# Performance work log

Hardware: AMD Instinct MI355X
Metric: run time of the kernel (lower is better)

Reference implementation:

```python
import jax, jax.numpy as jnp
import numpy as np

B, S, D = 4, 2048, 1024  # batch, seq_len, d_model (d_in == d_model)


def setup_inputs() -> dict:
    key = jax.random.key(0)
    ks = jax.random.split(key, 9)
    scale = 1.0 / np.sqrt(D)
    return {
        "q": jax.random.normal(ks[0], (B, S, D), jnp.float32),
        "k": jax.random.normal(ks[1], (B, S, D), jnp.float32),
        "v": jax.random.normal(ks[2], (B, S, D), jnp.float32),
        "Wq": jax.random.normal(ks[3], (D, D), jnp.float32) * scale,
        "bq": jnp.zeros((D,), jnp.float32),
        "Wk": jax.random.normal(ks[4], (D, D), jnp.float32) * scale,
        "bk": jnp.zeros((D,), jnp.float32),
        "Wv": jax.random.normal(ks[5], (D, D), jnp.float32) * scale,
        "bv": jnp.zeros((D,), jnp.float32),
    }


def reference(q, k, v, Wq, bq, Wk, bk, Wv, bv):
    query = q @ Wq + bq                      # [B, S, D]
    key_p = k @ Wk + bk                      # [B, S, D]
    value = v @ Wv + bv                      # [B, S, D]
    inv_sqrt_d = 1.0 / jnp.sqrt(jnp.asarray(D, query.dtype))
    scores = jnp.einsum('bqd,bkd->bqk', query, key_p) * inv_sqrt_d  # [B, S, S]
    w = jax.nn.softmax(scores, axis=-1)
    return jnp.einsum('bqk,bkd->bqd', w, value)  # [B, S, D]
```

## Files before the change

### kernel.cpp

```cpp
#include <hip/hip_runtime.h>
#include <math.h>


using short8  = __attribute__((ext_vector_type(8))) short;
using floatx4 = __attribute__((ext_vector_type(4))) float;

__device__ __forceinline__ unsigned short f2bf(float f) {
    union { float f; unsigned u; } x; x.f = f;
    return (unsigned short)((x.u + 0x8000u) >> 16);
}

__device__ __forceinline__ void gload_lds16(const unsigned short* g, unsigned short* l) {
    __builtin_amdgcn_global_load_lds(
        (const __attribute__((address_space(1))) unsigned int*)g,
        (__attribute__((address_space(3))) unsigned int*)l, 16, 0, 0);
}

#define SBAR   __builtin_amdgcn_s_barrier()
#define LGKM0  asm volatile("s_waitcnt lgkmcnt(0)" ::: "memory")
#define VMW(n) asm volatile("s_waitcnt vmcnt(" #n ")" ::: "memory")

__global__ __launch_bounds__(256) void prep(
    const float* __restrict__ q, const float* __restrict__ k, const float* __restrict__ v,
    const float* __restrict__ W0, const float* __restrict__ W1, const float* __restrict__ W2,
    unsigned short* __restrict__ qkvbf, unsigned short* __restrict__ Wt)
{
    __shared__ float tile[32][33];
    const int id = blockIdx.x;
    const int t  = threadIdx.x;
    if (id < 24576) {
        const int z  = id >> 13;
        const int xb = id & 8191;
        const float* x = (z == 0) ? q : (z == 1) ? k : v;
        const size_t i = ((size_t)xb * 256 + t) * 4;
        const float4 a = *(const float4*)(x + i);
        ushort4 p = { f2bf(a.x), f2bf(a.y), f2bf(a.z), f2bf(a.w) };
        *(ushort4*)(qkvbf + (size_t)z * 8192 * 1024 + i) = p;
    } else {
        const int idt = id - 24576;
        const int z  = idt >> 10;
        const int r  = idt & 1023;
        const int bx = (r & 31) * 32;
        const int by = (r >> 5) * 32;
        const float* W = (z == 0) ? W0 : (z == 1) ? W1 : W2;
        unsigned short* o = Wt + (size_t)z * 1024 * 1024;
        const int tx = t & 31;
        const int ty = (t >> 5) * 4;
        #pragma unroll
        for (int rr = 0; rr < 4; ++rr)
            tile[ty + rr][tx] = W[(size_t)(by + ty + rr) * 1024 + bx + tx];
        __syncthreads();
        #pragma unroll
        for (int rr = 0; rr < 4; ++rr)
            o[(size_t)(bx + ty + rr) * 1024 + by + tx] = f2bf(tile[tx][ty + rr]);
    }
}


#define STAGE_A(bb, kh, tt) do { \
    gload_lds16(gA + (size_t)srowA * lda + (tt) * 64 + (kh) * 32 + scol, \
                lds + (bb) * 24576 + (kh) * 4096 + t512 * 8); \
} while (0)

#define STAGE_B(bb, kh, tt) do { \
    const unsigned short* s_ = gB + (size_t)srowA * ldb + (tt) * 64 + (kh) * 32 + scol; \
    unsigned short* d_ = lds + (bb) * 24576 + 8192 + (kh) * 8192 + t512 * 8; \
    gload_lds16(s_, d_); \
    gload_lds16(s_ + (size_t)128 * ldb, d_ + 4096); \
} while (0)

#define LDSA(bb, kh, i) (*(const short8*)&lds[(bb) * 24576 + (kh) * 4096 + (arow + (i) * 16) * 32 + rslot])
#define LDSB(bb, kh, j) (*(const short8*)&lds[(bb) * 24576 + 8192 + (kh) * 8192 + (brow + (j) * 16) * 32 + rslot])

#define MFMA16 do { \
    __builtin_amdgcn_s_setprio(1); \
    _Pragma("unroll") \
    for (int i_ = 0; i_ < 4; ++i_) \
        _Pragma("unroll") \
        for (int j_ = 0; j_ < 4; ++j_) \
            acc[i_][j_] = __builtin_amdgcn_mfma_f32_16x16x32_bf16( \
                af[i_], bf[j_], acc[i_][j_], 0, 0, 0); \
    __builtin_amdgcn_s_setprio(0); \
} while (0)

__device__ __forceinline__ void gemm2ph(
    const unsigned short* __restrict__ gA, int lda,
    const unsigned short* __restrict__ gB, int ldb,
    int nt, unsigned short* lds, floatx4 (&acc)[4][4])
{
    const int t512 = threadIdx.x;
    const int lane = t512 & 63;
    const int wave = t512 >> 6;
    const int wr   = wave >> 2;
    const int wc   = wave & 3;
    const int l15  = lane & 15;
    const int quad = lane >> 4;
    const int srowA = t512 >> 2;
    const int scol  = ((t512 & 3) ^ ((t512 >> 3) & 3)) * 8;
    const int rslot = (quad ^ ((l15 >> 1) & 3)) * 8;
    const int arow  = wr * 64 + l15;
    const int brow  = wc * 64 + l15;

    short8 af[4], bf[4];

    STAGE_A(0, 0, 0); STAGE_B(0, 0, 0);
    STAGE_A(0, 1, 0); STAGE_B(0, 1, 0);
    STAGE_A(1, 0, 1); STAGE_B(1, 0, 1);
    VMW(6);
    SBAR;

    int b = 0;
    for (int t = 0; t < nt; ++t, b ^= 1) {
        #pragma unroll
        for (int j = 0; j < 4; ++j) bf[j] = LDSB(b, 0, j);
        #pragma unroll
        for (int i = 0; i < 4; ++i) af[i] = LDSA(b, 0, i);
        if (t + 1 < nt) { STAGE_A(b ^ 1, 1, t + 1); STAGE_B(b ^ 1, 1, t + 1); }
        SBAR; LGKM0;
        MFMA16;
        if (t < nt - 1) VMW(6); else VMW(0);
        SBAR;
        #pragma unroll
        for (int j = 0; j < 4; ++j) bf[j] = LDSB(b, 1, j);
        #pragma unroll
        for (int i = 0; i < 4; ++i) af[i] = LDSA(b, 1, i);
        if (t + 2 < nt) { STAGE_A(b, 0, t + 2); STAGE_B(b, 0, t + 2); }
        SBAR; LGKM0;
        MFMA16;
        if (t < nt - 1) {
            if (t + 2 < nt) VMW(6); else VMW(3);
            SBAR;
        }
    }
}

#define EPI_IDS                                   \
    const int tt   = threadIdx.x;                 \
    const int lane = tt & 63;                     \
    const int wave = tt >> 6;                     \
    const int wr   = wave >> 2;                   \
    const int wc   = wave & 3;                    \
    const int l15  = lane & 15;                   \
    const int quad = lane >> 4;

__global__ __launch_bounds__(512) void proj8(
    const unsigned short* __restrict__ Abf,
    const unsigned short* __restrict__ Wt,
    const float* __restrict__ bq, const float* __restrict__ bk, const float* __restrict__ bv,
    unsigned short* __restrict__ Qp, unsigned short* __restrict__ Kp,
    unsigned short* __restrict__ Vpt)
{
    __shared__ __attribute__((aligned(16))) unsigned short lds[49152];
    const int id = blockIdx.x;
    const int g  = (id & 7) * 96 + (id >> 3);
    const int z  = g >> 8;
    const int r  = g & 255;
    const int m0 = (r >> 2) * 128;
    const int n0 = (r & 3) * 256;

    const unsigned short* gA = Abf + (size_t)z * 8192 * 1024 + (size_t)m0 * 1024;
    const unsigned short* gB = Wt  + (size_t)z * 1024 * 1024 + (size_t)n0 * 1024;

    floatx4 acc[4][4] = {};
    gemm2ph(gA, 1024, gB, 1024, 16, lds, acc);

    EPI_IDS
    const float* bias = (z == 0) ? bq : (z == 1) ? bk : bv;
    #pragma unroll
    for (int j = 0; j < 4; ++j) {
        const int col = n0 + wc * 64 + j * 16 + l15;
        const float bv_ = bias[col];
        #pragma unroll
        for (int i = 0; i < 4; ++i) {
            const int row = m0 + wr * 64 + i * 16 + quad * 4;
            if (z < 2) {
                unsigned short* C = (z == 0) ? Qp : Kp;
                #pragma unroll
                for (int r2 = 0; r2 < 4; ++r2)
                    C[(size_t)(row + r2) * 1024 + col] = f2bf(acc[i][j][r2] + bv_);
            } else {
                ushort4 p = { f2bf(acc[i][j][0] + bv_), f2bf(acc[i][j][1] + bv_),
                              f2bf(acc[i][j][2] + bv_), f2bf(acc[i][j][3] + bv_) };
                *(ushort4*)&Vpt[(size_t)col * 8192 + row] = p;
            }
        }
    }
}

__global__ __launch_bounds__(512) void scores8(
    const unsigned short* __restrict__ Qp,
    const unsigned short* __restrict__ Kp,
    unsigned short* __restrict__ Pexp,
    float* __restrict__ rowsum)
{
    __shared__ __attribute__((aligned(16))) unsigned short lds[49152];
    const int id = blockIdx.x;
    const int g  = (id & 7) * 64 + (id >> 3);
    const int z  = g >> 7;
    const int r  = g & 127;
    const int m0 = (r >> 3) * 128;
    const int n0 = (r & 7) * 256;

    const unsigned short* gA = Qp + (size_t)z * 2048 * 1024 + (size_t)m0 * 1024;
    const unsigned short* gB = Kp + (size_t)z * 2048 * 1024 + (size_t)n0 * 1024;

    floatx4 acc[4][4] = {};
    gemm2ph(gA, 1024, gB, 1024, 16, lds, acc);

    EPI_IDS
    unsigned short* P = Pexp + (size_t)z * 2048 * 2048;
    float* rs = rowsum + (size_t)z * 2048;
    #pragma unroll
    for (int i = 0; i < 4; ++i) {
        const int rowb = m0 + wr * 64 + i * 16 + quad * 4;
        float sm[4] = {0.f, 0.f, 0.f, 0.f};
        #pragma unroll
        for (int j = 0; j < 4; ++j) {
            const int col = n0 + wc * 64 + j * 16 + l15;
            #pragma unroll
            for (int r2 = 0; r2 < 4; ++r2) {
                const float p = __expf(acc[i][j][r2] * 0.03125f);
                sm[r2] += p;
                P[(size_t)(rowb + r2) * 2048 + col] = f2bf(p);
            }
        }
        #pragma unroll
        for (int r2 = 0; r2 < 4; ++r2) {
            float s = sm[r2];
            s += __shfl_xor(s, 1);
            s += __shfl_xor(s, 2);
            s += __shfl_xor(s, 4);
            s += __shfl_xor(s, 8);
            if (l15 == 0)
                atomicAdd(&rs[rowb + r2], s);
        }
    }
}

__global__ __launch_bounds__(512) void pv8(
    const unsigned short* __restrict__ Pexp,
    const unsigned short* __restrict__ Vpt,
    const float* __restrict__ rowsum,
    float* __restrict__ out)
{
    __shared__ __attribute__((aligned(16))) unsigned short lds[49152];
    const int id = blockIdx.x;
    const int g  = (id & 7) * 32 + (id >> 3);
    const int z  = g >> 6;
    const int r  = g & 63;
    const int m0 = (r >> 2) * 128;
    const int n0 = (r & 3) * 256;

    const unsigned short* gA = Pexp + (size_t)z * 2048 * 2048 + (size_t)m0 * 2048;
    const unsigned short* gB = Vpt  + (size_t)n0 * 8192 + (size_t)z * 2048;

    floatx4 acc[4][4] = {};
    gemm2ph(gA, 2048, gB, 8192, 32, lds, acc);

    EPI_IDS
    const float* rs = rowsum + (size_t)z * 2048;
    float* C = out + (size_t)z * 2048 * 1024;
    #pragma unroll
    for (int i = 0; i < 4; ++i) {
        const int rowb = m0 + wr * 64 + i * 16 + quad * 4;
        float inv[4];
        #pragma unroll
        for (int r2 = 0; r2 < 4; ++r2) inv[r2] = 1.0f / rs[rowb + r2];
        #pragma unroll
        for (int j = 0; j < 4; ++j) {
            const int col = n0 + wc * 64 + j * 16 + l15;
            #pragma unroll
            for (int r2 = 0; r2 < 4; ++r2)
                C[(size_t)(rowb + r2) * 1024 + col] = acc[i][j][r2] * inv[r2];
        }
    }
}

extern "C" void kernel_launch(void* const* d_in, const int* in_sizes, int n_in,
                              void* d_out, int out_size, void* d_ws, size_t ws_size,
                              hipStream_t stream)
{
    const float* q  = (const float*)d_in[0];
    const float* k  = (const float*)d_in[1];
    const float* v  = (const float*)d_in[2];
    const float* Wq = (const float*)d_in[3];
    const float* bq = (const float*)d_in[4];
    const float* Wk = (const float*)d_in[5];
    const float* bk = (const float*)d_in[6];
    const float* Wv = (const float*)d_in[7];
    const float* bv = (const float*)d_in[8];
    float* out = (float*)d_out;

    const int Bn = 4, S = 2048;

    char* w = (char*)d_ws;
    unsigned short* Wt     = (unsigned short*)(w);
    unsigned short* Qp     = (unsigned short*)(w + (6u << 20));
    unsigned short* Kp     = (unsigned short*)(w + (22u << 20));
    unsigned short* Vpt    = (unsigned short*)(w + (38u << 20));
    unsigned short* qkvbf  = (unsigned short*)(w + (54u << 20));
    unsigned short* Pexp   = (unsigned short*)(w + (54u << 20));
    float*          rowsum = (float*)(w + (86u << 20));

    hipMemsetAsync(rowsum, 0, (size_t)Bn * S * sizeof(float), stream);

    prep<<<dim3(27648), dim3(256), 0, stream>>>(q, k, v, Wq, Wk, Wv, qkvbf, Wt);

    proj8<<<dim3(768), dim3(512), 0, stream>>>(qkvbf, Wt, bq, bk, bv, Qp, Kp, Vpt);

    scores8<<<dim3(512), dim3(512), 0, stream>>>(Qp, Kp, Pexp, rowsum);

    pv8<<<dim3(256), dim3(512), 0, stream>>>(Pexp, Vpt, rowsum, out);
}
```

Baseline: 310.2 us.

## Triple-buffer LDS in shared GEMM mainloop for deeper prefetch

```diff
diff --git a/kernel.cpp b/kernel.cpp
--- a/kernel.cpp
+++ b/kernel.cpp
@@ -83,7 +83,7 @@
     __builtin_amdgcn_s_setprio(0); \
 } while (0)
 
-__device__ __forceinline__ void gemm2ph(
+__device__ __forceinline__ void gemm3buf(
     const unsigned short* __restrict__ gA, int lda,
     const unsigned short* __restrict__ gB, int ldb,
     int nt, unsigned short* lds, floatx4 (&acc)[4][4])
@@ -106,31 +106,35 @@
     STAGE_A(0, 0, 0); STAGE_B(0, 0, 0);
     STAGE_A(0, 1, 0); STAGE_B(0, 1, 0);
     STAGE_A(1, 0, 1); STAGE_B(1, 0, 1);
-    VMW(6);
+    STAGE_A(1, 1, 1); STAGE_B(1, 1, 1);
+    VMW(9);
     SBAR;
 
-    int b = 0;
-    for (int t = 0; t < nt; ++t, b ^= 1) {
-        #pragma unroll
-        for (int j = 0; j < 4; ++j) bf[j] = LDSB(b, 0, j);
-        #pragma unroll
-        for (int i = 0; i < 4; ++i) af[i] = LDSA(b, 0, i);
-        if (t + 1 < nt) { STAGE_A(b ^ 1, 1, t + 1); STAGE_B(b ^ 1, 1, t + 1); }
+    int b0 = 0, b1 = 1, b2 = 2;
+    for (int t = 0; t < nt; ++t) {
+        #pragma unroll
+        for (int j = 0; j < 4; ++j) bf[j] = LDSB(b0, 0, j);
+        #pragma unroll
+        for (int i = 0; i < 4; ++i) af[i] = LDSA(b0, 0, i);
+        if (t + 2 < nt) { STAGE_A(b2, 0, t + 2); STAGE_B(b2, 0, t + 2); }
         SBAR; LGKM0;
         MFMA16;
-        if (t < nt - 1) VMW(6); else VMW(0);
+        if (t < nt - 2)       { VMW(9); }
+        else if (t == nt - 2) { VMW(6); }
+        else                  { VMW(0); }
         SBAR;
         #pragma unroll
-        for (int j = 0; j < 4; ++j) bf[j] = LDSB(b, 1, j);
-        #pragma unroll
-        for (int i = 0; i < 4; ++i) af[i] = LDSA(b, 1, i);
-        if (t + 2 < nt) { STAGE_A(b, 0, t + 2); STAGE_B(b, 0, t + 2); }
+        for (int j = 0; j < 4; ++j) bf[j] = LDSB(b0, 1, j);
+        #pragma unroll
+        for (int i = 0; i < 4; ++i) af[i] = LDSA(b0, 1, i);
+        if (t + 2 < nt) { STAGE_A(b2, 1, t + 2); STAGE_B(b2, 1, t + 2); }
         SBAR; LGKM0;
         MFMA16;
         if (t < nt - 1) {
-            if (t + 2 < nt) VMW(6); else VMW(3);
+            if (t < nt - 2) { VMW(9); } else { VMW(3); }
             SBAR;
         }
+        const int tmp = b0; b0 = b1; b1 = b2; b2 = tmp;
     }
 }
 
@@ -150,7 +154,7 @@
     unsigned short* __restrict__ Qp, unsigned short* __restrict__ Kp,
     unsigned short* __restrict__ Vpt)
 {
-    __shared__ __attribute__((aligned(16))) unsigned short lds[49152];
+    __shared__ __attribute__((aligned(16))) unsigned short lds[73728];
     const int id = blockIdx.x;
     const int g  = (id & 7) * 96 + (id >> 3);
     const int z  = g >> 8;
@@ -162,7 +166,7 @@
     const unsigned short* gB = Wt  + (size_t)z * 1024 * 1024 + (size_t)n0 * 1024;
 
     floatx4 acc[4][4] = {};
-    gemm2ph(gA, 1024, gB, 1024, 16, lds, acc);
+    gemm3buf(gA, 1024, gB, 1024, 16, lds, acc);
 
     EPI_IDS
     const float* bias = (z == 0) ? bq : (z == 1) ? bk : bv;
@@ -193,7 +197,7 @@
     unsigned short* __restrict__ Pexp,
     float* __restrict__ rowsum)
 {
-    __shared__ __attribute__((aligned(16))) unsigned short lds[49152];
+    __shared__ __attribute__((aligned(16))) unsigned short lds[73728];
     const int id = blockIdx.x;
     const int g  = (id & 7) * 64 + (id >> 3);
     const int z  = g >> 7;
@@ -205,7 +209,7 @@
     const unsigned short* gB = Kp + (size_t)z * 2048 * 1024 + (size_t)n0 * 1024;
 
     floatx4 acc[4][4] = {};
-    gemm2ph(gA, 1024, gB, 1024, 16, lds, acc);
+    gemm3buf(gA, 1024, gB, 1024, 16, lds, acc);
 
     EPI_IDS
     unsigned short* P = Pexp + (size_t)z * 2048 * 2048;
@@ -243,7 +247,7 @@
     const float* __restrict__ rowsum,
     float* __restrict__ out)
 {
-    __shared__ __attribute__((aligned(16))) unsigned short lds[49152];
+    __shared__ __attribute__((aligned(16))) unsigned short lds[73728];
     const int id = blockIdx.x;
     const int g  = (id & 7) * 32 + (id >> 3);
     const int z  = g >> 6;
@@ -255,7 +259,7 @@
     const unsigned short* gB = Vpt  + (size_t)n0 * 8192 + (size_t)z * 2048;
 
     floatx4 acc[4][4] = {};
-    gemm2ph(gA, 2048, gB, 8192, 32, lds, acc);
+    gemm3buf(gA, 2048, gB, 8192, 32, lds, acc);
 
     EPI_IDS
     const float* rs = rowsum + (size_t)z * 2048;
```

Measured after the change: 302.8 us. 1.02x faster.
